# Optimization experiments

Hardware: AMD Instinct MI355X
Metric: run time of the kernel (lower is better)

Reference implementation:

```python
import jax, jax.numpy as jnp
import numpy as np

B, CIN, COUT, H, W = 16, 512, 128, 64, 64


def setup_inputs() -> dict:
    key = jax.random.key(0)
    k1, k2, k3 = jax.random.split(key, 3)
    x = jax.random.normal(k1, (B, CIN, H, W), dtype=jnp.float32)
    style = jax.random.normal(k2, (B, CIN), dtype=jnp.float32)
    # kaiming_normal_ on [COUT, CIN, 1, 1]: fan_in = CIN*1*1, std = sqrt(2/fan_in)
    weight = jax.random.normal(k3, (COUT, CIN), dtype=jnp.float32) * np.float32(np.sqrt(2.0 / CIN))
    return {"x": x, "style": style, "weight": weight}


def reference(x, style, weight):
    # Per-sample modulated weight: mw[b,o,c] = style[b,c] * weight[o,c]
    # 1x1 conv, padding=0, stride=1 -> batched channel-mixing GEMM:
    # out[b,o,h,w] = sum_c mw[b,o,c] * x[b,c,h,w]
    return jnp.einsum('oc,bc,bchw->bohw', weight, style, x)
```

## Files before the change

kernel.cpp:

```cpp
#include <hip/hip_runtime.h>
#include <stdint.h>

#define NB    16
#define CIN   512
#define COUT  128
#define HW    4096
#define BN    64
#define BK    32
#define NIT   (CIN / BK)
#define NTILES (HW / BN)

using bf16x8  = __attribute__((ext_vector_type(8))) __bf16;
using floatx4 = __attribute__((ext_vector_type(4))) float;

__device__ __forceinline__ unsigned short f2bf_bits(float f) {
    union { float f; unsigned u; } v; v.f = f;
    return (unsigned short)((v.u + 0x7fffu + ((v.u >> 16) & 1u)) >> 16);
}

#define GLD16(g, l)                                                            \
    __builtin_amdgcn_global_load_lds(                                          \
        (const __attribute__((address_space(1))) void*)(g),                    \
        (__attribute__((address_space(3))) void*)(l), 16, 0, 0)

__global__ __launch_bounds__(256)
void modw_kernel(const float* __restrict__ style,
                 const float* __restrict__ weight,
                 __bf16* __restrict__ mw)
{
    const int id = blockIdx.x * 256 + threadIdx.x;
    const int k8 = id & 63;
    const int m  = (id >> 6) & 127;
    const int b  = id >> 13;

    const float4 w0 = *(const float4*)(weight + m * CIN + k8 * 8);
    const float4 w1 = *(const float4*)(weight + m * CIN + k8 * 8 + 4);
    const float4 s0 = *(const float4*)(style + b * CIN + k8 * 8);
    const float4 s1 = *(const float4*)(style + b * CIN + k8 * 8 + 4);

    union { unsigned short us[8]; bf16x8 v; } pk;
    pk.us[0] = f2bf_bits(w0.x * s0.x);
    pk.us[1] = f2bf_bits(w0.y * s0.y);
    pk.us[2] = f2bf_bits(w0.z * s0.z);
    pk.us[3] = f2bf_bits(w0.w * s0.w);
    pk.us[4] = f2bf_bits(w1.x * s1.x);
    pk.us[5] = f2bf_bits(w1.y * s1.y);
    pk.us[6] = f2bf_bits(w1.z * s1.z);
    pk.us[7] = f2bf_bits(w1.w * s1.w);
    *(bf16x8*)(mw + ((size_t)(b * 64 + k8) * 128 + m) * 8) = pk.v;
}

__global__ __launch_bounds__(256, 4)
void modconv1x1_kernel(const float* __restrict__ x,
                       const __bf16* __restrict__ mw,
                       float* __restrict__ out)
{
    __shared__ __align__(16) __bf16 Alds[2][(BK / 8) * COUT * 8];
    __shared__ __align__(16) __bf16 Blds[2][(BK / 8) * BN * 8];

    const int tid = threadIdx.x;
    const int b   = blockIdx.x >> 6;
    const int n0  = (blockIdx.x & 63) * BN;

    const float* xb   = x   + (size_t)b * CIN * HW + n0;
    float*       outb = out + (size_t)b * COUT * HW + n0;
    const char*  mwb  = (const char*)mw + (size_t)b * (64 * 128 * 16);

    const int lane = tid & 63;
    const int wave = tid >> 6;
    const int quad = lane >> 4;
    const int l15  = lane & 15;
    const int wm   = (wave & 1) * 64;
    const int wn   = (wave >> 1) * 32;

    const int bn_ = lane;
    const int bk8 = wave;

    floatx4 acc[4][2];
    #pragma unroll
    for (int i = 0; i < 4; ++i)
        #pragma unroll
        for (int j = 0; j < 2; ++j)
            acc[i][j] = (floatx4){0.f, 0.f, 0.f, 0.f};

    {
        const char* t  = mwb;
        char*       al = (char*)&Alds[0][0];
        GLD16(t + wave * 2048 + lane * 16,        al + wave * 2048);
        GLD16(t + wave * 2048 + 1024 + lane * 16, al + wave * 2048 + 1024);

        const float* src = xb + (size_t)(bk8 * 8) * HW + bn_;
        float rb[8];
        #pragma unroll
        for (int j = 0; j < 8; ++j) rb[j] = src[(size_t)j * HW];
        union { unsigned short us[8]; bf16x8 v; } pk;
        #pragma unroll
        for (int j = 0; j < 8; ++j) pk.us[j] = f2bf_bits(rb[j]);
        *(bf16x8*)&Blds[0][(bk8 * BN + bn_) * 8] = pk.v;
    }

    int cur = 0;
    for (int it = 0; it < NIT; ++it) {
        __syncthreads();

        float rb[8];
        if (it + 1 < NIT) {
            const int knext = (it + 1) * BK;
            const char* t  = mwb + (size_t)knext * 256;
            char*       al = (char*)&Alds[cur ^ 1][0];
            GLD16(t + wave * 2048 + lane * 16,        al + wave * 2048);
            GLD16(t + wave * 2048 + 1024 + lane * 16, al + wave * 2048 + 1024);
            const float* src = xb + (size_t)(knext + bk8 * 8) * HW + bn_;
            #pragma unroll
            for (int j = 0; j < 8; ++j) rb[j] = src[(size_t)j * HW];
        }

        bf16x8 af[4], bfr[2];
        #pragma unroll
        for (int tm = 0; tm < 4; ++tm)
            af[tm] = *(const bf16x8*)&Alds[cur][(quad * COUT + wm + tm * 16 + l15) * 8];
        #pragma unroll
        for (int tn = 0; tn < 2; ++tn)
            bfr[tn] = *(const bf16x8*)&Blds[cur][(quad * BN + wn + tn * 16 + l15) * 8];
        #pragma unroll
        for (int tm = 0; tm < 4; ++tm)
            #pragma unroll
            for (int tn = 0; tn < 2; ++tn)
                acc[tm][tn] = __builtin_amdgcn_mfma_f32_16x16x32_bf16(
                    af[tm], bfr[tn], acc[tm][tn], 0, 0, 0);

        if (it + 1 < NIT) {
            union { unsigned short us[8]; bf16x8 v; } pk;
            #pragma unroll
            for (int j = 0; j < 8; ++j) pk.us[j] = f2bf_bits(rb[j]);
            *(bf16x8*)&Blds[cur ^ 1][(bk8 * BN + bn_) * 8] = pk.v;
        }
        cur ^= 1;
    }

    #pragma unroll
    for (int tm = 0; tm < 4; ++tm) {
        const int o = wm + tm * 16 + quad * 4;
        #pragma unroll
        for (int tn = 0; tn < 2; ++tn) {
            const int n = wn + tn * 16 + l15;
            #pragma unroll
            for (int r = 0; r < 4; ++r)
                outb[(size_t)(o + r) * HW + n] = acc[tm][tn][r];
        }
    }
}

extern "C" void kernel_launch(void* const* d_in, const int* in_sizes, int n_in,
                              void* d_out, int out_size, void* d_ws, size_t ws_size,
                              hipStream_t stream) {
    const float* x      = (const float*)d_in[0];
    const float* style  = (const float*)d_in[1];
    const float* weight = (const float*)d_in[2];
    float* out = (float*)d_out;
    __bf16* mw = (__bf16*)d_ws;

    modw_kernel<<<dim3(512), dim3(256), 0, stream>>>(style, weight, mw);
    modconv1x1_kernel<<<dim3(NB * NTILES), dim3(256), 0, stream>>>(x, mw, out);
}
```

Baseline: 213.0 us.

## Drop LDS staging; load MFMA operands directly from global into registers per wave

Removes the shared-memory double buffers and block-wide barriers from the GEMM. Each wave now owns a 64x32 output tile and loads its A fragments and x columns straight from global memory into a register double buffer. This is meant to remove LDS traffic and __syncthreads stalls. In exchange there is no reuse of operands across the waves of a block, so x is read twice (once per M-half), global accesses are narrower, and register pressure rises.

```diff
diff --git a/kernel.cpp b/kernel.cpp
--- a/kernel.cpp
+++ b/kernel.cpp
@@ -5,10 +5,7 @@
 #define CIN   512
 #define COUT  128
 #define HW    4096
-#define BN    64
-#define BK    32
-#define NIT   (CIN / BK)
-#define NTILES (HW / BN)
+#define NIT   16
 
 using bf16x8  = __attribute__((ext_vector_type(8))) __bf16;
 using floatx4 = __attribute__((ext_vector_type(4))) float;
@@ -17,11 +14,6 @@
     union { float f; unsigned u; } v; v.f = f;
     return (unsigned short)((v.u + 0x7fffu + ((v.u >> 16) & 1u)) >> 16);
 }
-
-#define GLD16(g, l)                                                            \
-    __builtin_amdgcn_global_load_lds(                                          \
-        (const __attribute__((address_space(1))) void*)(g),                    \
-        (__attribute__((address_space(3))) void*)(l), 16, 0, 0)
 
 __global__ __launch_bounds__(256)
 void modw_kernel(const float* __restrict__ style,
@@ -55,26 +47,21 @@
                        const __bf16* __restrict__ mw,
                        float* __restrict__ out)
 {
-    __shared__ __align__(16) __bf16 Alds[2][(BK / 8) * COUT * 8];
-    __shared__ __align__(16) __bf16 Blds[2][(BK / 8) * BN * 8];
-
-    const int tid = threadIdx.x;
-    const int b   = blockIdx.x >> 6;
-    const int n0  = (blockIdx.x & 63) * BN;
-
-    const float* xb   = x   + (size_t)b * CIN * HW + n0;
-    float*       outb = out + (size_t)b * COUT * HW + n0;
-    const char*  mwb  = (const char*)mw + (size_t)b * (64 * 128 * 16);
-
+    const int tid  = threadIdx.x;
     const int lane = tid & 63;
     const int wave = tid >> 6;
     const int quad = lane >> 4;
     const int l15  = lane & 15;
-    const int wm   = (wave & 1) * 64;
-    const int wn   = (wave >> 1) * 32;
 
-    const int bn_ = lane;
-    const int bk8 = wave;
+    const int b     = blockIdx.x >> 6;
+    const int idx   = (blockIdx.x & 63) * 4 + wave;
+    const int mhalf = idx & 1;
+    const int n0    = (idx >> 1) * 32;
+    const int wm    = mhalf * 64;
+
+    const float*  xb   = x   + (size_t)b * CIN * HW + n0;
+    float*        outb = out + (size_t)b * COUT * HW + n0;
+    const __bf16* mwb  = mw  + (size_t)b * (64 * 128 * 8);
 
     floatx4 acc[4][2];
     #pragma unroll
@@ -83,67 +70,53 @@
         for (int j = 0; j < 2; ++j)
             acc[i][j] = (floatx4){0.f, 0.f, 0.f, 0.f};
 
-    {
-        const char* t  = mwb;
-        char*       al = (char*)&Alds[0][0];
-        GLD16(t + wave * 2048 + lane * 16,        al + wave * 2048);
-        GLD16(t + wave * 2048 + 1024 + lane * 16, al + wave * 2048 + 1024);
+    bf16x8 afA[2][4];
+    float  rbf[2][16];
 
-        const float* src = xb + (size_t)(bk8 * 8) * HW + bn_;
-        float rb[8];
-        #pragma unroll
-        for (int j = 0; j < 8; ++j) rb[j] = src[(size_t)j * HW];
-        union { unsigned short us[8]; bf16x8 v; } pk;
-        #pragma unroll
-        for (int j = 0; j < 8; ++j) pk.us[j] = f2bf_bits(rb[j]);
-        *(bf16x8*)&Blds[0][(bk8 * BN + bn_) * 8] = pk.v;
+#define LOAD_STAGE(S, ST)                                                      \
+    {                                                                          \
+        const __bf16* abase = mwb + (size_t)((4 * (S) + quad) * 128) * 8;      \
+        _Pragma("unroll")                                                      \
+        for (int tm = 0; tm < 4; ++tm)                                         \
+            afA[ST][tm] = *(const bf16x8*)(abase + (wm + tm * 16 + l15) * 8);  \
+        const float* src = xb + (size_t)((4 * (S) + quad) * 8) * HW + l15;     \
+        _Pragma("unroll")                                                      \
+        for (int tn = 0; tn < 2; ++tn)                                         \
+            _Pragma("unroll")                                                  \
+            for (int j = 0; j < 8; ++j)                                        \
+                rbf[ST][tn * 8 + j] = src[(size_t)j * HW + tn * 16];           \
     }
 
-    int cur = 0;
-    for (int it = 0; it < NIT; ++it) {
-        __syncthreads();
+    LOAD_STAGE(0, 0)
 
-        float rb[8];
-        if (it + 1 < NIT) {
-            const int knext = (it + 1) * BK;
-            const char* t  = mwb + (size_t)knext * 256;
-            char*       al = (char*)&Alds[cur ^ 1][0];
-            GLD16(t + wave * 2048 + lane * 16,        al + wave * 2048);
-            GLD16(t + wave * 2048 + 1024 + lane * 16, al + wave * 2048 + 1024);
-            const float* src = xb + (size_t)(knext + bk8 * 8) * HW + bn_;
+    for (int s = 0; s < NIT; ++s) {
+        const int cur = s & 1;
+        if (s + 1 < NIT) LOAD_STAGE(s + 1, cur ^ 1)
+
+        bf16x8 bfr[2];
+        #pragma unroll
+        for (int tn = 0; tn < 2; ++tn) {
+            union { unsigned short us[8]; bf16x8 v; } pk;
             #pragma unroll
-            for (int j = 0; j < 8; ++j) rb[j] = src[(size_t)j * HW];
+            for (int j = 0; j < 8; ++j)
+                pk.us[j] = f2bf_bits(rbf[cur][tn * 8 + j]);
+            bfr[tn] = pk.v;
         }
-
-        bf16x8 af[4], bfr[2];
-        #pragma unroll
-        for (int tm = 0; tm < 4; ++tm)
-            af[tm] = *(const bf16x8*)&Alds[cur][(quad * COUT + wm + tm * 16 + l15) * 8];
-        #pragma unroll
-        for (int tn = 0; tn < 2; ++tn)
-            bfr[tn] = *(const bf16x8*)&Blds[cur][(quad * BN + wn + tn * 16 + l15) * 8];
         #pragma unroll
         for (int tm = 0; tm < 4; ++tm)
             #pragma unroll
             for (int tn = 0; tn < 2; ++tn)
                 acc[tm][tn] = __builtin_amdgcn_mfma_f32_16x16x32_bf16(
-                    af[tm], bfr[tn], acc[tm][tn], 0, 0, 0);
-
-        if (it + 1 < NIT) {
-            union { unsigned short us[8]; bf16x8 v; } pk;
-            #pragma unroll
-            for (int j = 0; j < 8; ++j) pk.us[j] = f2bf_bits(rb[j]);
-            *(bf16x8*)&Blds[cur ^ 1][(bk8 * BN + bn_) * 8] = pk.v;
-        }
-        cur ^= 1;
+                    afA[cur][tm], bfr[tn], acc[tm][tn], 0, 0, 0);
     }
+#undef LOAD_STAGE
 
     #pragma unroll
     for (int tm = 0; tm < 4; ++tm) {
         const int o = wm + tm * 16 + quad * 4;
         #pragma unroll
         for (int tn = 0; tn < 2; ++tn) {
-            const int n = wn + tn * 16 + l15;
+            const int n = tn * 16 + l15;
             #pragma unroll
             for (int r = 0; r < 4; ++r)
                 outb[(size_t)(o + r) * HW + n] = acc[tm][tn][r];
@@ -161,5 +134,5 @@
     __bf16* mw = (__bf16*)d_ws;
 
     modw_kernel<<<dim3(512), dim3(256), 0, stream>>>(style, weight, mw);
-    modconv1x1_kernel<<<dim3(NB * NTILES), dim3(256), 0, stream>>>(x, mw, out);
+    modconv1x1_kernel<<<dim3(NB * 64), dim3(256), 0, stream>>>(x, mw, out);
 }
```

After: 218.8 us. 1.03x slower.
